# Kernel tuning notes

Measured on AMD Instinct MI355X. Metric: run time of the kernel, lower is better.

The kernel has to match this reference:

```python
import jax, jax.numpy as jnp
import numpy as np

EPS = 1e-12  # F.normalize eps


def quat2matrix(J):
    # J: [B, N, D, 4] in (x, y, z, w) order; normalized then reordered to (w, x, y, z)
    norm = jnp.sqrt(jnp.sum(J * J, axis=-1, keepdims=True))
    Jn = J / jnp.maximum(norm, EPS)
    x, y, z, w = Jn[..., 0], Jn[..., 1], Jn[..., 2], Jn[..., 3]
    # pytorch3d quaternion_to_matrix with q = (r, i, j, k) = (w, x, y, z)
    two_s = 2.0 / (w * w + x * x + y * y + z * z)
    r00 = 1.0 - two_s * (y * y + z * z)
    r01 = two_s * (x * y - z * w)
    r02 = two_s * (x * z + y * w)
    r10 = two_s * (x * y + z * w)
    r11 = 1.0 - two_s * (x * x + z * z)
    r12 = two_s * (y * z - x * w)
    r20 = two_s * (x * z - y * w)
    r21 = two_s * (y * z + x * w)
    r22 = 1.0 - two_s * (x * x + y * y)
    R = jnp.stack([
        jnp.stack([r00, r01, r02], axis=-1),
        jnp.stack([r10, r11, r12], axis=-1),
        jnp.stack([r20, r21, r22], axis=-1),
    ], axis=-2)  # [B, N, D, 3, 3]
    return R


def setup_inputs() -> dict:
    key = jax.random.key(0)
    k1, k2, k3, k4, k5 = jax.random.split(key, 5)
    Bb, N, D, F = 8, 4096, 256, 256  # batch, points, in_channels, out_channels
    return {
        "X": jax.random.normal(k1, (Bb, N, D, 3), dtype=jnp.float32),
        "J": jax.random.normal(k2, (Bb, N, D, 4), dtype=jnp.float32),
        "A": jax.random.normal(k3, (F, D), dtype=jnp.float32),
        "B": jax.random.normal(k4, (F, D), dtype=jnp.float32),
        "C": jax.random.normal(k5, (F, D), dtype=jnp.float32),
    }


def reference(X, J, A, B, C):
    R = quat2matrix(J)  # [B, N, D, 3, 3]
    # RTX[..., i] = (R^T X)_i = sum_k R[..., k, i] * X[..., k]
    RTX = jnp.einsum('bndki,bndk->bndi', R, X)  # [B, N, D, 3]
    rt0 = RTX[..., 0:1]
    rt1 = RTX[..., 1:2]
    rt2 = RTX[..., 2:3]
    # get_rrtx(i, R, s) = R[..., :, i] * s (column i of R scaled by scalar)
    a_term = R[..., :, 0] * rt0 + R[..., :, 1] * rt1  # [B, N, D, 3]
    b_term = R[..., :, 1] * rt0 - R[..., :, 0] * rt1
    c_term = R[..., :, 2] * rt2
    Y = (jnp.einsum('fe,bnei->bnfi', A, a_term)
         + jnp.einsum('fe,bnei->bnfi', B, b_term)
         + jnp.einsum('fe,bnei->bnfi', C, c_term))  # [B, N, F, 3]
    return Y
```

## Files before the change

### kernel.cpp

```cpp
#include <hip/hip_runtime.h>


typedef __bf16 bf16_t;
typedef __attribute__((ext_vector_type(8))) __bf16 bf16x8;
typedef __attribute__((ext_vector_type(4))) __bf16 bf16x4;
typedef __attribute__((ext_vector_type(4))) float f32x4;

constexpr int Dd    = 256;
constexpr int Gp    = 16;
constexpr int TPB   = 512;
constexpr int PITCH = 776;

__device__ __forceinline__ bf16_t to_bf16(float f) {
    unsigned u = __builtin_bit_cast(unsigned, f);
    u += 0x7FFFu + ((u >> 16) & 1u);
    unsigned short h = (unsigned short)(u >> 16);
    return __builtin_bit_cast(bf16_t, h);
}

__global__ __launch_bounds__(256)
void convert_w_kernel(const float* __restrict__ A, const float* __restrict__ B,
                      const float* __restrict__ C, bf16_t* __restrict__ W)
{
    const int e4 = (blockIdx.x * 256 + threadIdx.x) * 4;
    const float* src;
    if (e4 < 65536)        src = A + e4;
    else if (e4 < 131072)  src = B + (e4 - 65536);
    else                   src = C + (e4 - 131072);
    const float4 v = *reinterpret_cast<const float4*>(src);
    bf16x4 o;
    o[0] = to_bf16(v.x); o[1] = to_bf16(v.y); o[2] = to_bf16(v.z); o[3] = to_bf16(v.w);
    *reinterpret_cast<bf16x4*>(W + e4) = o;
}

__global__ __launch_bounds__(TPB)
void alaq_mfma_kernel(const float* __restrict__ X, const float* __restrict__ J,
                      const bf16_t* __restrict__ W, float* __restrict__ Y)
{
    __shared__ bf16_t TT[48 * PITCH];

    const int tid = threadIdx.x;
    const long bn0 = (long)blockIdx.x * Gp;

    #pragma unroll
    for (int rr = 0; rr < 8; ++rr) {
        const int idx = rr * TPB + tid;
        const int p = idx >> 8;
        const int e = idx & 255;
        const long base = (bn0 + p) * Dd + e;

        const float4 q = *reinterpret_cast<const float4*>(J + base * 4);
        const float* xp = X + base * 3;
        const float x0 = xp[0], x1 = xp[1], x2 = xp[2];

        const float nsq = q.x*q.x + q.y*q.y + q.z*q.z + q.w*q.w;
        const float inv = 1.0f / fmaxf(sqrtf(nsq), 1e-12f);
        const float qx = q.x*inv, qy = q.y*inv, qz = q.z*inv, qw = q.w*inv;
        const float s = 2.0f / (qw*qw + qx*qx + qy*qy + qz*qz);

        const float r00 = 1.0f - s*(qy*qy + qz*qz);
        const float r01 = s*(qx*qy - qz*qw);
        const float r02 = s*(qx*qz + qy*qw);
        const float r10 = s*(qx*qy + qz*qw);
        const float r11 = 1.0f - s*(qx*qx + qz*qz);
        const float r12 = s*(qy*qz - qx*qw);
        const float r20 = s*(qx*qz - qy*qw);
        const float r21 = s*(qy*qz + qx*qw);
        const float r22 = 1.0f - s*(qx*qx + qy*qy);

        const float rt0 = r00*x0 + r10*x1 + r20*x2;
        const float rt1 = r01*x0 + r11*x1 + r21*x2;
        const float rt2 = r02*x0 + r12*x1 + r22*x2;

        const int row = (p * 3) * PITCH;
        TT[row             + e      ] = to_bf16(r00*rt0 + r01*rt1);
        TT[row +     PITCH + e      ] = to_bf16(r10*rt0 + r11*rt1);
        TT[row + 2 * PITCH + e      ] = to_bf16(r20*rt0 + r21*rt1);
        TT[row             + 256 + e] = to_bf16(r01*rt0 - r00*rt1);
        TT[row +     PITCH + 256 + e] = to_bf16(r11*rt0 - r10*rt1);
        TT[row + 2 * PITCH + 256 + e] = to_bf16(r21*rt0 - r20*rt1);
        TT[row             + 512 + e] = to_bf16(r02*rt2);
        TT[row +     PITCH + 512 + e] = to_bf16(r12*rt2);
        TT[row + 2 * PITCH + 512 + e] = to_bf16(r22*rt2);
    }
    __syncthreads();

    const int w  = tid >> 6;
    const int l  = tid & 63;
    const int lr = l & 15;
    const int lq = l >> 4;

    f32x4 acc[3][2] = {};

    const int f0 = (2 * w    ) * 16 + lr;
    const int f1 = (2 * w + 1) * 16 + lr;

    #pragma unroll 4
    for (int k0 = 0; k0 < 24; ++k0) {
        const int term = k0 >> 3;
        const int eb   = ((k0 & 7) << 5) + (lq << 3);
        const bf16x8 b0 = *reinterpret_cast<const bf16x8*>(W + (term << 16) + f0 * 256 + eb);
        const bf16x8 b1 = *reinterpret_cast<const bf16x8*>(W + (term << 16) + f1 * 256 + eb);

        const int kcol = (k0 << 5) + (lq << 3);
        const bf16x8 a0 = *reinterpret_cast<const bf16x8*>(&TT[( 0 + lr) * PITCH + kcol]);
        const bf16x8 a1 = *reinterpret_cast<const bf16x8*>(&TT[(16 + lr) * PITCH + kcol]);
        const bf16x8 a2 = *reinterpret_cast<const bf16x8*>(&TT[(32 + lr) * PITCH + kcol]);

        acc[0][0] = __builtin_amdgcn_mfma_f32_16x16x32_bf16(a0, b0, acc[0][0], 0, 0, 0);
        acc[1][0] = __builtin_amdgcn_mfma_f32_16x16x32_bf16(a1, b0, acc[1][0], 0, 0, 0);
        acc[2][0] = __builtin_amdgcn_mfma_f32_16x16x32_bf16(a2, b0, acc[2][0], 0, 0, 0);
        acc[0][1] = __builtin_amdgcn_mfma_f32_16x16x32_bf16(a0, b1, acc[0][1], 0, 0, 0);
        acc[1][1] = __builtin_amdgcn_mfma_f32_16x16x32_bf16(a1, b1, acc[1][1], 0, 0, 0);
        acc[2][1] = __builtin_amdgcn_mfma_f32_16x16x32_bf16(a2, b1, acc[2][1], 0, 0, 0);
    }

    #pragma unroll
    for (int mi = 0; mi < 3; ++mi) {
        #pragma unroll
        for (int ni = 0; ni < 2; ++ni) {
            const int f = (2 * w + ni) * 16 + lr;
            #pragma unroll
            for (int r = 0; r < 4; ++r) {
                const int m = mi * 16 + lq * 4 + r;
                const int p = m / 3;
                const int i = m - p * 3;
                Y[(bn0 + p) * 768 + f * 3 + i] = acc[mi][ni][r];
            }
        }
    }
}

extern "C" void kernel_launch(void* const* d_in, const int* in_sizes, int n_in,
                              void* d_out, int out_size, void* d_ws, size_t ws_size,
                              hipStream_t stream) {
    const float* X  = (const float*)d_in[0];
    const float* J  = (const float*)d_in[1];
    const float* A  = (const float*)d_in[2];
    const float* B  = (const float*)d_in[3];
    const float* Cm = (const float*)d_in[4];
    float* Y = (float*)d_out;
    bf16_t* W = (bf16_t*)d_ws;

    convert_w_kernel<<<192, 256, 0, stream>>>(A, B, Cm, W);

    const int nbn = in_sizes[1] / (Dd * 4);
    const int blocks = nbn / Gp;
    alaq_mfma_kernel<<<blocks, TPB, 0, stream>>>(X, J, W, Y);
}
```

Before: 161.4 us.

## Swizzle shared tile layout, batch global loads upfront, and fully unroll MFMA loop

Replaces the padded LDS pitch with an unpadded 768-wide layout using an XOR swizzle on the k index to avoid bank conflicts. All J and X loads for a thread are issued before any compute so more memory requests are in flight. The MFMA k-loop is fully unrolled with precomputed W pointers, and launch bounds now request 4 blocks per SM. This adds register pressure from holding 8 quaternions and positions, which may spill or limit occupancy.

```diff
diff --git a/kernel.cpp b/kernel.cpp
--- a/kernel.cpp
+++ b/kernel.cpp
@@ -6,16 +6,19 @@
 typedef __attribute__((ext_vector_type(4))) __bf16 bf16x4;
 typedef __attribute__((ext_vector_type(4))) float f32x4;
 
-constexpr int Dd    = 256;
-constexpr int Gp    = 16;
-constexpr int TPB   = 512;
-constexpr int PITCH = 776;
+constexpr int Dd  = 256;
+constexpr int Gp  = 16;
+constexpr int TPB = 512;
 
 __device__ __forceinline__ bf16_t to_bf16(float f) {
     unsigned u = __builtin_bit_cast(unsigned, f);
     u += 0x7FFFu + ((u >> 16) & 1u);
     unsigned short h = (unsigned short)(u >> 16);
     return __builtin_bit_cast(bf16_t, h);
+}
+
+__device__ __forceinline__ int swz(int row, int k) {
+    return row * 768 + (k ^ ((row & 7) << 3));
 }
 
 __global__ __launch_bounds__(256)
@@ -33,25 +36,34 @@
     *reinterpret_cast<bf16x4*>(W + e4) = o;
 }
 
-__global__ __launch_bounds__(TPB)
+__global__ __launch_bounds__(TPB, 4)
 void alaq_mfma_kernel(const float* __restrict__ X, const float* __restrict__ J,
                       const bf16_t* __restrict__ W, float* __restrict__ Y)
 {
-    __shared__ bf16_t TT[48 * PITCH];
+    __shared__ bf16_t TT[48 * 768];
 
     const int tid = threadIdx.x;
     const long bn0 = (long)blockIdx.x * Gp;
+    const long ebase = bn0 * Dd;
+
+    float4 qv[8];
+    float  xv[8][3];
+    #pragma unroll
+    for (int rr = 0; rr < 8; ++rr) {
+        const long base = ebase + rr * TPB + tid;
+        qv[rr] = *reinterpret_cast<const float4*>(J + base * 4);
+        const float* xp = X + base * 3;
+        xv[rr][0] = xp[0]; xv[rr][1] = xp[1]; xv[rr][2] = xp[2];
+    }
 
     #pragma unroll
     for (int rr = 0; rr < 8; ++rr) {
         const int idx = rr * TPB + tid;
         const int p = idx >> 8;
         const int e = idx & 255;
-        const long base = (bn0 + p) * Dd + e;
 
-        const float4 q = *reinterpret_cast<const float4*>(J + base * 4);
-        const float* xp = X + base * 3;
-        const float x0 = xp[0], x1 = xp[1], x2 = xp[2];
+        const float4 q = qv[rr];
+        const float x0 = xv[rr][0], x1 = xv[rr][1], x2 = xv[rr][2];
 
         const float nsq = q.x*q.x + q.y*q.y + q.z*q.z + q.w*q.w;
         const float inv = 1.0f / fmaxf(sqrtf(nsq), 1e-12f);
@@ -72,16 +84,16 @@
         const float rt1 = r01*x0 + r11*x1 + r21*x2;
         const float rt2 = r02*x0 + r12*x1 + r22*x2;
 
-        const int row = (p * 3) * PITCH;
-        TT[row             + e      ] = to_bf16(r00*rt0 + r01*rt1);
-        TT[row +     PITCH + e      ] = to_bf16(r10*rt0 + r11*rt1);
-        TT[row + 2 * PITCH + e      ] = to_bf16(r20*rt0 + r21*rt1);
-        TT[row             + 256 + e] = to_bf16(r01*rt0 - r00*rt1);
-        TT[row +     PITCH + 256 + e] = to_bf16(r11*rt0 - r10*rt1);
-        TT[row + 2 * PITCH + 256 + e] = to_bf16(r21*rt0 - r20*rt1);
-        TT[row             + 512 + e] = to_bf16(r02*rt2);
-        TT[row +     PITCH + 512 + e] = to_bf16(r12*rt2);
-        TT[row + 2 * PITCH + 512 + e] = to_bf16(r22*rt2);
+        const int row = p * 3;
+        TT[swz(row    ,       e)] = to_bf16(r00*rt0 + r01*rt1);
+        TT[swz(row + 1,       e)] = to_bf16(r10*rt0 + r11*rt1);
+        TT[swz(row + 2,       e)] = to_bf16(r20*rt0 + r21*rt1);
+        TT[swz(row    , 256 + e)] = to_bf16(r01*rt0 - r00*rt1);
+        TT[swz(row + 1, 256 + e)] = to_bf16(r11*rt0 - r10*rt1);
+        TT[swz(row + 2, 256 + e)] = to_bf16(r21*rt0 - r20*rt1);
+        TT[swz(row    , 512 + e)] = to_bf16(r02*rt2);
+        TT[swz(row + 1, 512 + e)] = to_bf16(r12*rt2);
+        TT[swz(row + 2, 512 + e)] = to_bf16(r22*rt2);
     }
     __syncthreads();
 
@@ -92,20 +104,22 @@
 
     f32x4 acc[3][2] = {};
 
-    const int f0 = (2 * w    ) * 16 + lr;
-    const int f1 = (2 * w + 1) * 16 + lr;
+    const int f0 = (2 * w) * 16 + lr;
+    const bf16_t* Wf0 = W + f0 * 256 + (lq << 3);
+    const bf16_t* Wf1 = Wf0 + 16 * 256;
+    const int swzmask = (lr & 7) << 3;
 
-    #pragma unroll 4
+    #pragma unroll
     for (int k0 = 0; k0 < 24; ++k0) {
         const int term = k0 >> 3;
-        const int eb   = ((k0 & 7) << 5) + (lq << 3);
-        const bf16x8 b0 = *reinterpret_cast<const bf16x8*>(W + (term << 16) + f0 * 256 + eb);
-        const bf16x8 b1 = *reinterpret_cast<const bf16x8*>(W + (term << 16) + f1 * 256 + eb);
+        const int eb   = (k0 & 7) << 5;
+        const bf16x8 b0 = *reinterpret_cast<const bf16x8*>(Wf0 + (term << 16) + eb);
+        const bf16x8 b1 = *reinterpret_cast<const bf16x8*>(Wf1 + (term << 16) + eb);
 
-        const int kcol = (k0 << 5) + (lq << 3);
-        const bf16x8 a0 = *reinterpret_cast<const bf16x8*>(&TT[( 0 + lr) * PITCH + kcol]);
-        const bf16x8 a1 = *reinterpret_cast<const bf16x8*>(&TT[(16 + lr) * PITCH + kcol]);
-        const bf16x8 a2 = *reinterpret_cast<const bf16x8*>(&TT[(32 + lr) * PITCH + kcol]);
+        const int kswz = (((k0 << 5) + (lq << 3)) ^ swzmask);
+        const bf16x8 a0 = *reinterpret_cast<const bf16x8*>(&TT[         lr  * 768 + kswz]);
+        const bf16x8 a1 = *reinterpret_cast<const bf16x8*>(&TT[(16 +    lr) * 768 + kswz]);
+        const bf16x8 a2 = *reinterpret_cast<const bf16x8*>(&TT[(32 +    lr) * 768 + kswz]);
 
         acc[0][0] = __builtin_amdgcn_mfma_f32_16x16x32_bf16(a0, b0, acc[0][0], 0, 0, 0);
         acc[1][0] = __builtin_amdgcn_mfma_f32_16x16x32_bf16(a1, b0, acc[1][0], 0, 0, 0);
```

New measurement: 144.5 us. 1.12x faster.
